# Optimization experiments

Measured on AMD Instinct MI355X. Metric: run time of the kernel, lower is better.

Reference implementation:

```python
import jax, jax.numpy as jnp
import numpy as np

F_NODE = 32   # node feature dim
E_ATTR = 8    # edge attribute dim
H_OUT = 64    # h_theta output dim


def setup_inputs() -> dict:
    key = jax.random.key(0)
    k1, k2, k3 = jax.random.split(key, 3)
    B, N = 1, 1024
    adjacency = jax.random.randint(k1, (B, N, N), 0, 2, dtype=jnp.int32)
    node_features = jax.random.normal(k2, (B, N, F_NODE), dtype=jnp.float32)
    edge_attributes = jax.random.normal(k3, (B, N, N, E_ATTR), dtype=jnp.float32)
    kW = jax.random.fold_in(key, 7)
    W = jax.random.normal(kW, (2 * F_NODE + E_ATTR, H_OUT), dtype=jnp.float32) * (1.0 / np.sqrt(2 * F_NODE + E_ATTR))
    b = jnp.zeros((H_OUT,), dtype=jnp.float32)
    return {"adjacency": adjacency, "node_features": node_features,
            "edge_attributes": edge_attributes, "W": W, "b": b}


def reference(adjacency, node_features, edge_attributes, W, b):
    # EdgeConvE: per edge (v, v') compute h_theta(concat([x_v, x_v' - x_v, e_vv']))
    # then aggregate over neighbors v' selected by the dense adjacency.
    # Split W along the concat axis so we never materialize the [B,N,N,2F+E] concat:
    # concat @ W = x_v @ W_self + (x_v' - x_v) @ W_diff + e @ W_edge
    F = node_features.shape[-1]
    W_self, W_diff, W_edge = W[:F], W[F:2 * F], W[2 * F:]
    self_term = node_features @ (W_self - W_diff)            # [B,N,H]
    nbr_term = node_features @ W_diff                        # [B,N,H]
    edge_term = jnp.einsum('bvwe,eh->bvwh', edge_attributes, W_edge)  # [B,N,N,H]
    msg = jax.nn.relu(self_term[:, :, None, :] + nbr_term[:, None, :, :] + edge_term + b)
    A = adjacency.astype(msg.dtype)                          # [B,N,N] 0/1 mask
    out = jnp.einsum('bvw,bvwh->bvh', A, msg)                # sum-aggregate over neighbors
    return out
```

## Files before the change

kernel.cpp:

```cpp
#include <hip/hip_runtime.h>
#include <hip/hip_bf16.h>

#define N 1024
#define F 32
#define H 64
#define EA 8

typedef __attribute__((ext_vector_type(8))) short bf16x8;
typedef __attribute__((ext_vector_type(16))) float f32x16;

union FragAB { bf16x8 v; unsigned u[4]; };

__device__ __forceinline__ unsigned pk(float a, float b) {
    union { __hip_bfloat162 h; unsigned u; } c;
    c.h = __float22bfloat162_rn(float2{a, b});
    return c.u;
}

__global__ __launch_bounds__(256) void precompute_terms(
    const float* __restrict__ X, const float* __restrict__ W, const float* __restrict__ b,
    float* __restrict__ sv, float* __restrict__ nb, float* __restrict__ out)
{
    const int lane = threadIdx.x & 63;
    const int wid  = threadIdx.x >> 6;
    const int v    = blockIdx.x * 4 + wid;

    float4 xr[8];
    const float4* xp = (const float4*)(X + (size_t)v * F);
#pragma unroll
    for (int i = 0; i < 8; ++i) xr[i] = xp[i];
    const float* xf = (const float*)xr;

    float s = b[lane];
    float n = 0.f;
#pragma unroll
    for (int f = 0; f < F; ++f) {
        float ws = W[f * H + lane];
        float wd = W[(F + f) * H + lane];
        s = fmaf(xf[f], ws - wd, s);
        n = fmaf(xf[f], wd, n);
    }
    const int idx = v * H + lane;
    sv[idx]  = s;
    nb[idx]  = n;
    out[idx] = 0.f;
}

__global__ __launch_bounds__(256, 4) void edge_mfma(
    const int* __restrict__ A, const float* __restrict__ Edge, const float* __restrict__ W,
    const float* __restrict__ sv, const float* __restrict__ nb, float* __restrict__ out)
{
    const int lane = threadIdx.x & 63;
    const int wid  = threadIdx.x >> 6;
    const int lg   = lane >> 5;
    const int ln   = lane & 31;
    const int wq   = blockIdx.x & 7;
    const int vch  = blockIdx.x >> 3;
    const int wbase = wq * 128 + wid * 32;
    const int vbase = vch * 8;

    __shared__ float part[4][2][8][64];

    const int* ap = A + (size_t)vbase * N + wbase + ln;
    int am[8]; float s0v[8], s1v[8];
#pragma unroll
    for (int vi = 0; vi < 8; ++vi) {
        am[vi]  = ap[(size_t)vi * N];
        s0v[vi] = sv[(size_t)(vbase + vi) * H + ln];
        s1v[vi] = sv[(size_t)(vbase + vi) * H + 32 + ln];
    }

    const float4* ep = (const float4*)(Edge + ((size_t)vbase * N + wbase + ln) * EA);
    float4 eA[2], eB[2];
    eA[0] = ep[0];    eB[0] = ep[1];
    eA[1] = ep[2048]; eB[1] = ep[2049];

    FragAB bfr[2];
#pragma unroll
    for (int half = 0; half < 2; ++half) {
        const int n = half * 32 + ln;
#pragma unroll
        for (int q = 0; q < 4; ++q) {
            unsigned we = pk(W[(2 * F + 2 * q) * H + n], W[(2 * F + 2 * q + 1) * H + n]);
            bfr[half].u[q] = (lg == 0) ? we : 0u;
        }
    }

    f32x16 cnb[2];
#pragma unroll
    for (int half = 0; half < 2; ++half)
#pragma unroll
        for (int r = 0; r < 16; ++r) {
            const int row = (r & 3) + 8 * (r >> 2) + 4 * lg;
            cnb[half][r] = nb[(size_t)(wbase + row) * H + half * 32 + ln];
        }

#pragma unroll
    for (int vi = 0; vi < 8; ++vi) {
        const float4 ca = eA[vi & 1];
        const float4 cb = eB[vi & 1];
        if (vi < 6) {
            eA[vi & 1] = ep[(vi + 2) * 2048];
            eB[vi & 1] = ep[(vi + 2) * 2048 + 1];
        }

        FragAB afr;
        const unsigned mpat = am[vi] ? 0x00003f80u : 0xbf803f80u;
        afr.u[0] = (lg == 0) ? pk(ca.x, ca.y) : mpat;
        afr.u[1] = (lg == 0) ? pk(ca.z, ca.w) : 0u;
        afr.u[2] = (lg == 0) ? pk(cb.x, cb.y) : 0u;
        afr.u[3] = (lg == 0) ? pk(cb.z, cb.w) : 0u;

        FragAB b0 = bfr[0], b1 = bfr[1];
        if (lg) { b0.u[0] = pk(s0v[vi], 1e30f); b1.u[0] = pk(s1v[vi], 1e30f); }

        const f32x16 d0 = __builtin_amdgcn_mfma_f32_32x32x16_bf16(afr.v, b0.v, cnb[0], 0, 0, 0);
        const f32x16 d1 = __builtin_amdgcn_mfma_f32_32x32x16_bf16(afr.v, b1.v, cnb[1], 0, 0, 0);

        float p0 = 0.f, p1 = 0.f;
#pragma unroll
        for (int r = 0; r < 16; ++r) {
            p0 += fmaxf(d0[r], 0.f);
            p1 += fmaxf(d1[r], 0.f);
        }
        part[wid][lg][vi][ln]      = p0;
        part[wid][lg][vi][32 + ln] = p1;
    }

    __syncthreads();
#pragma unroll
    for (int i = threadIdx.x; i < 512; i += 256) {
        const int vi = i >> 6, h = i & 63;
        float s = 0.f;
#pragma unroll
        for (int w4 = 0; w4 < 4; ++w4)
#pragma unroll
            for (int g = 0; g < 2; ++g) s += part[w4][g][vi][h];
        unsafeAtomicAdd(&out[(size_t)(vbase + vi) * H + h], s);
    }
}

extern "C" void kernel_launch(void* const* d_in, const int* in_sizes, int n_in,
                              void* d_out, int out_size, void* d_ws, size_t ws_size,
                              hipStream_t stream) {
    const int*   A    = (const int*)d_in[0];
    const float* X    = (const float*)d_in[1];
    const float* Edge = (const float*)d_in[2];
    const float* W    = (const float*)d_in[3];
    const float* b    = (const float*)d_in[4];
    float* out = (float*)d_out;

    float* sv = (float*)d_ws;
    float* nb = sv + N * H;

    precompute_terms<<<dim3(256), dim3(256), 0, stream>>>(X, W, b, sv, nb, out);
    edge_mfma<<<dim3(1024), dim3(256), 0, stream>>>(A, Edge, W, sv, nb, out);
}
```

Before: 89.29 us.

## Pre-swizzle neighbor and self terms into MFMA fragment layout

The precompute kernel now writes the self term already packed as bf16 pairs with the 1e30 sentinel, and writes the neighbor term in the accumulator register layout the MFMA expects. The edge kernel can then load its accumulator init with contiguous float4 loads instead of 32 strided scalar loads. Loads of the adjacency, self term, edge and W are also predicated so each lane half only fetches what it uses. This cuts redundant and uncoalesced global traffic at the cost of more complex index math and lane-divergent branches.

```diff
diff --git a/kernel.cpp b/kernel.cpp
--- a/kernel.cpp
+++ b/kernel.cpp
@@ -19,7 +19,7 @@
 
 __global__ __launch_bounds__(256) void precompute_terms(
     const float* __restrict__ X, const float* __restrict__ W, const float* __restrict__ b,
-    float* __restrict__ sv, float* __restrict__ nb, float* __restrict__ out)
+    uint2* __restrict__ svq, float* __restrict__ nbL, float* __restrict__ out)
 {
     const int lane = threadIdx.x & 63;
     const int wid  = threadIdx.x >> 6;
@@ -40,15 +40,23 @@
         s = fmaf(xf[f], ws - wd, s);
         n = fmaf(xf[f], wd, n);
     }
-    const int idx = v * H + lane;
-    sv[idx]  = s;
-    nb[idx]  = n;
-    out[idx] = 0.f;
+    out[v * H + lane] = 0.f;
+
+    const unsigned p  = pk(s, 1e30f);
+    const unsigned ph = __shfl_down(p, 32);
+    if (lane < 32) svq[v * 32 + lane] = uint2{p, ph};
+
+    const int t  = v >> 5, w5 = v & 31;
+    const int lg = (w5 >> 2) & 1;
+    const int r  = (w5 & 3) + 4 * (w5 >> 3);
+    const int hh = lane >> 5;
+    const int l  = (lane & 31) | (lg << 5);
+    nbL[(((t * 2 + hh) * 64 + l) << 4) + r] = n;
 }
 
 __global__ __launch_bounds__(256, 4) void edge_mfma(
     const int* __restrict__ A, const float* __restrict__ Edge, const float* __restrict__ W,
-    const float* __restrict__ sv, const float* __restrict__ nb, float* __restrict__ out)
+    const uint2* __restrict__ svq, const float* __restrict__ nbL, float* __restrict__ out)
 {
     const int lane = threadIdx.x & 63;
     const int wid  = threadIdx.x >> 6;
@@ -58,61 +66,72 @@
     const int vch  = blockIdx.x >> 3;
     const int wbase = wq * 128 + wid * 32;
     const int vbase = vch * 8;
+    const int t     = wq * 4 + wid;
 
     __shared__ float part[4][2][8][64];
 
-    const int* ap = A + (size_t)vbase * N + wbase + ln;
-    int am[8]; float s0v[8], s1v[8];
+    int am[8]; uint2 sq[8];
+    if (lg) {
+        const int* ap = A + (size_t)vbase * N + wbase + ln;
 #pragma unroll
-    for (int vi = 0; vi < 8; ++vi) {
-        am[vi]  = ap[(size_t)vi * N];
-        s0v[vi] = sv[(size_t)(vbase + vi) * H + ln];
-        s1v[vi] = sv[(size_t)(vbase + vi) * H + 32 + ln];
+        for (int vi = 0; vi < 8; ++vi) {
+            am[vi] = ap[(size_t)vi * N];
+            sq[vi] = svq[(vbase + vi) * 32 + ln];
+        }
     }
 
     const float4* ep = (const float4*)(Edge + ((size_t)vbase * N + wbase + ln) * EA);
     float4 eA[2], eB[2];
-    eA[0] = ep[0];    eB[0] = ep[1];
-    eA[1] = ep[2048]; eB[1] = ep[2049];
+    if (!lg) {
+        eA[0] = ep[0];    eB[0] = ep[1];
+        eA[1] = ep[2048]; eB[1] = ep[2049];
+    }
 
     FragAB bfr[2];
 #pragma unroll
-    for (int half = 0; half < 2; ++half) {
-        const int n = half * 32 + ln;
+    for (int half = 0; half < 2; ++half)
 #pragma unroll
-        for (int q = 0; q < 4; ++q) {
-            unsigned we = pk(W[(2 * F + 2 * q) * H + n], W[(2 * F + 2 * q + 1) * H + n]);
-            bfr[half].u[q] = (lg == 0) ? we : 0u;
+        for (int q = 0; q < 4; ++q) bfr[half].u[q] = 0u;
+    if (!lg) {
+#pragma unroll
+        for (int half = 0; half < 2; ++half) {
+            const int n = half * 32 + ln;
+#pragma unroll
+            for (int q = 0; q < 4; ++q)
+                bfr[half].u[q] = pk(W[(2 * F + 2 * q) * H + n], W[(2 * F + 2 * q + 1) * H + n]);
         }
     }
 
     f32x16 cnb[2];
 #pragma unroll
-    for (int half = 0; half < 2; ++half)
+    for (int hh = 0; hh < 2; ++hh) {
+        const float4* cp = (const float4*)(nbL + (((t * 2 + hh) * 64 + lane) << 4));
 #pragma unroll
-        for (int r = 0; r < 16; ++r) {
-            const int row = (r & 3) + 8 * (r >> 2) + 4 * lg;
-            cnb[half][r] = nb[(size_t)(wbase + row) * H + half * 32 + ln];
+        for (int q = 0; q < 4; ++q) {
+            const float4 x = cp[q];
+            cnb[hh][4 * q + 0] = x.x; cnb[hh][4 * q + 1] = x.y;
+            cnb[hh][4 * q + 2] = x.z; cnb[hh][4 * q + 3] = x.w;
         }
+    }
 
 #pragma unroll
     for (int vi = 0; vi < 8; ++vi) {
         const float4 ca = eA[vi & 1];
         const float4 cb = eB[vi & 1];
-        if (vi < 6) {
+        if (vi < 6 && !lg) {
             eA[vi & 1] = ep[(vi + 2) * 2048];
             eB[vi & 1] = ep[(vi + 2) * 2048 + 1];
         }
 
         FragAB afr;
         const unsigned mpat = am[vi] ? 0x00003f80u : 0xbf803f80u;
-        afr.u[0] = (lg == 0) ? pk(ca.x, ca.y) : mpat;
-        afr.u[1] = (lg == 0) ? pk(ca.z, ca.w) : 0u;
-        afr.u[2] = (lg == 0) ? pk(cb.x, cb.y) : 0u;
-        afr.u[3] = (lg == 0) ? pk(cb.z, cb.w) : 0u;
+        afr.u[0] = lg ? mpat : pk(ca.x, ca.y);
+        afr.u[1] = lg ? 0u : pk(ca.z, ca.w);
+        afr.u[2] = lg ? 0u : pk(cb.x, cb.y);
+        afr.u[3] = lg ? 0u : pk(cb.z, cb.w);
 
         FragAB b0 = bfr[0], b1 = bfr[1];
-        if (lg) { b0.u[0] = pk(s0v[vi], 1e30f); b1.u[0] = pk(s1v[vi], 1e30f); }
+        if (lg) { b0.u[0] = sq[vi].x; b1.u[0] = sq[vi].y; }
 
         const f32x16 d0 = __builtin_amdgcn_mfma_f32_32x32x16_bf16(afr.v, b0.v, cnb[0], 0, 0, 0);
         const f32x16 d1 = __builtin_amdgcn_mfma_f32_32x32x16_bf16(afr.v, b1.v, cnb[1], 0, 0, 0);
@@ -150,9 +169,9 @@
     const float* b    = (const float*)d_in[4];
     float* out = (float*)d_out;
 
-    float* sv = (float*)d_ws;
-    float* nb = sv + N * H;
+    uint2* svq = (uint2*)d_ws;
+    float* nbL = (float*)((char*)d_ws + N * 32 * sizeof(uint2));
 
-    precompute_terms<<<dim3(256), dim3(256), 0, stream>>>(X, W, b, sv, nb, out);
-    edge_mfma<<<dim3(1024), dim3(256), 0, stream>>>(A, Edge, W, sv, nb, out);
+    precompute_terms<<<dim3(256), dim3(256), 0, stream>>>(X, W, b, svq, nbL, out);
+    edge_mfma<<<dim3(1024), dim3(256), 0, stream>>>(A, Edge, W, svq, nbL, out);
 }
```

Result: slower. 98.80 us (+10.6%).
